# Optimization experiments

Hardware: AMD Instinct MI355X
Metric: run time of the kernel (lower is better)

The kernel has to match this reference:

```python
import jax, jax.numpy as jnp
import numpy as np

N_BATCH = 128   # C: number of PWL channels / generator batch
N_PTS = 32768   # N: samples per channel
K_PWL = 20      # breakpoints per piecewise-linear function
LATENT = 8
HID = 8
EPS = 1e-7


def _mlp(z, W1, b1, W2, b2):
    # torch mlp: Linear -> Tanh -> Linear -> Tanh
    h = jnp.tanh(z @ W1 + b1)
    return jnp.tanh(h @ W2 + b2)


def _normalize01(a):
    # per-row min/max normalization, a: [C, N]
    a = a - a.min(axis=1, keepdims=True)
    return a / a.max(axis=1, keepdims=True)


def _calibrate1d(x, xp, yp):
    # x: [N, C], xp/yp: [C, K]
    N, C = x.shape
    K = xp.shape[1]
    bp = jnp.concatenate([x[:, :, None], jnp.broadcast_to(xp[None], (N, C, K))], axis=2)  # [N,C,K+1]
    order = jnp.argsort(bp, axis=2)                       # [N,C,K+1]
    sorted_bp = jnp.take_along_axis(bp, order, axis=2)
    x_idx = jnp.argmin(order, axis=2)                     # rank of x among breakpoints
    cand = x_idx - 1
    start_idx = jnp.where(x_idx == 0, 1, jnp.where(x_idx == K, K - 2, cand))
    end_idx = jnp.where(start_idx == cand, start_idx + 2, start_idx + 1)
    start_x = jnp.take_along_axis(sorted_bp, start_idx[..., None], axis=2)[..., 0]
    end_x = jnp.take_along_axis(sorted_bp, end_idx[..., None], axis=2)[..., 0]
    start_idx2 = jnp.where(x_idx == 0, 0, jnp.where(x_idx == K, K - 2, cand))
    yp_e = jnp.broadcast_to(yp[None], (N, C, K))
    start_y = jnp.take_along_axis(yp_e, start_idx2[..., None], axis=2)[..., 0]
    end_y = jnp.take_along_axis(yp_e, (start_idx2 + 1)[..., None], axis=2)[..., 0]
    return start_y + (x - start_x) * (end_y - start_y) / (end_x - start_x + EPS)


def setup_inputs() -> dict:
    key = jax.random.key(0)
    ks = jax.random.split(key, 16)
    s = 0.5
    f32 = jnp.float32
    return {
        "zf": jax.random.normal(ks[0], (N_BATCH, LATENT), f32),
        "zx": jax.random.normal(ks[1], (N_BATCH, N_PTS, LATENT), f32),
        "ze": jax.random.normal(ks[2], (N_BATCH, N_PTS, LATENT), f32),
        "Wx1": jax.random.normal(ks[3], (LATENT, HID), f32) * s,
        "bx1": jax.random.normal(ks[4], (HID,), f32) * s,
        "Wx2": jax.random.normal(ks[5], (HID, 1), f32) * s,
        "bx2": jax.random.normal(ks[6], (1,), f32) * s,
        "We1": jax.random.normal(ks[7], (LATENT, HID), f32) * s,
        "be1": jax.random.normal(ks[8], (HID,), f32) * s,
        "We2": jax.random.normal(ks[9], (HID, 1), f32) * s,
        "be2": jax.random.normal(ks[10], (1,), f32) * s,
        "Wf1": jax.random.normal(ks[11], (LATENT, HID), f32) * s,
        "bf1": jax.random.normal(ks[12], (HID,), f32) * s,
        "Wf2": jax.random.normal(ks[13], (HID, K_PWL), f32) * s,
        "bf2": jax.random.normal(ks[14], (K_PWL,), f32) * s,
        "directions": jax.random.randint(ks[15], (N_BATCH,), 0, 2) > 0,
    }


def reference(zf, zx, ze, Wx1, bx1, Wx2, bx2, We1, be1, We2, be2, Wf1, bf1, Wf2, bf2, directions):
    # gen_f: random ascending/descending monotone PWL per channel
    pts = _mlp(zf, Wf1, bf1, Wf2, bf2)                        # [C, K]
    asc = jnp.sort(pts, axis=1)
    yp = jnp.where(directions[:, None], asc, asc[:, ::-1])    # [C, K]
    xp = jnp.broadcast_to(jnp.linspace(0.0, 1.0, K_PWL, dtype=pts.dtype)[None, :], yp.shape)
    # forward_x: cause variable, per-channel normalized to [0,1]
    x = _mlp(zx, Wx1, bx1, Wx2, bx2)[..., 0]                  # [C, N]
    x = _normalize01(x).T                                     # [N, C]
    # forward_e: standardized noise (global mean / unbiased std)
    e = _mlp(ze, We1, be1, We2, be2)[..., 0].T                # [N, C]
    e = (e - e.mean()) / e.std(ddof=1)
    # forward_y
    y = _calibrate1d(x, xp, yp) + 0.1 * e                     # [N, C]
    return y
```

## Files before the change

kernel.cpp:

```cpp
#include <hip/hip_runtime.h>

#define C_CH  128
#define NP    32768
#define K_PWL 20
#define LAT   8
#define HID   8
#define SLOTS 32

__device__ __forceinline__ float fast_tanh(float x) {
    float e = __expf(2.0f * x);
    return 1.0f - 2.0f / (e + 1.0f);
}

__device__ __forceinline__ unsigned fenc(float f) {
    unsigned u = __float_as_uint(f);
    return (u & 0x80000000u) ? ~u : (u | 0x80000000u);
}
__device__ __forceinline__ float fdec(unsigned e) {
    unsigned u = (e & 0x80000000u) ? (e ^ 0x80000000u) : ~e;
    return __uint_as_float(u);
}

__global__ void init_stats(unsigned* cminE, unsigned* cmaxE, double* sums) {
    int t = threadIdx.x;
    if (t < C_CH) { cminE[t] = 0xFFFFFFFFu; cmaxE[t] = 0u; }
    if (t < 2 * SLOTS) sums[t] = 0.0;
}

__global__ void gen_yp(const float* __restrict__ zf,
                       const float* __restrict__ Wf1, const float* __restrict__ bf1,
                       const float* __restrict__ Wf2, const float* __restrict__ bf2,
                       const unsigned char* __restrict__ dirs_raw,
                       float* __restrict__ ypw) {
    int c = threadIdx.x;
    __shared__ int is_i32;
    if (c == 0) {
        const int* di = (const int*)dirs_raw;
        int ok = 1;
        for (int i = 0; i < 32; i++) { int v = di[i]; if (v != 0 && v != 1) ok = 0; }
        is_i32 = ok;
    }
    __syncthreads();
    if (c >= C_CH) return;

    float z[LAT];
    #pragma unroll
    for (int l = 0; l < LAT; l++) z[l] = zf[c * LAT + l];
    float h[HID];
    #pragma unroll
    for (int j = 0; j < HID; j++) {
        float a = bf1[j];
        #pragma unroll
        for (int l = 0; l < LAT; l++) a = fmaf(z[l], Wf1[l * HID + j], a);
        h[j] = fast_tanh(a);
    }
    float p[K_PWL];
    #pragma unroll
    for (int k = 0; k < K_PWL; k++) {
        float a = bf2[k];
        #pragma unroll
        for (int j = 0; j < HID; j++) a = fmaf(h[j], Wf2[j * K_PWL + k], a);
        p[k] = fast_tanh(a);
    }
    for (int i = 1; i < K_PWL; i++) {
        float key = p[i];
        int j = i - 1;
        while (j >= 0 && p[j] > key) { p[j + 1] = p[j]; j--; }
        p[j + 1] = key;
    }
    int dir = is_i32 ? (((const int*)dirs_raw)[c] != 0) : (dirs_raw[c] != 0);
    for (int k = 0; k < K_PWL; k++)
        ypw[c * K_PWL + k] = dir ? p[k] : p[K_PWL - 1 - k];
}

__global__ __launch_bounds__(256)
void pass1(const float* __restrict__ zx, const float* __restrict__ ze,
           const float* __restrict__ Wx1, const float* __restrict__ bx1,
           const float* __restrict__ Wx2, const float* __restrict__ bx2,
           const float* __restrict__ We1, const float* __restrict__ be1,
           const float* __restrict__ We2, const float* __restrict__ be2,
           float* __restrict__ xraw, float* __restrict__ eraw,
           unsigned* __restrict__ cminE, unsigned* __restrict__ cmaxE,
           double* __restrict__ sums) {
    __shared__ float sw[162];
    int t = threadIdx.x;
    if (t < 64)       sw[t] = Wx1[t];
    else if (t < 72)  sw[t] = bx1[t - 64];
    else if (t < 80)  sw[t] = Wx2[t - 72];
    else if (t == 80) sw[80] = bx2[0];
    else if (t < 145) sw[t] = We1[t - 81];
    else if (t < 153) sw[t] = be1[t - 145];
    else if (t < 161) sw[t] = We2[t - 153];
    else if (t == 161) sw[161] = be2[0];
    __syncthreads();

    int c = blockIdx.y;
    int n = blockIdx.x * 256 + t;
    size_t base = ((size_t)c * NP + n) * LAT;

    const float4* zxp = (const float4*)(zx + base);
    float4 a0 = zxp[0], a1 = zxp[1];
    const float4* zep = (const float4*)(ze + base);
    float4 b0 = zep[0], b1 = zep[1];

    float xacc = sw[80];
    #pragma unroll
    for (int j = 0; j < HID; j++) {
        float hh = sw[64 + j];
        hh = fmaf(a0.x, sw[0 * 8 + j], hh);
        hh = fmaf(a0.y, sw[1 * 8 + j], hh);
        hh = fmaf(a0.z, sw[2 * 8 + j], hh);
        hh = fmaf(a0.w, sw[3 * 8 + j], hh);
        hh = fmaf(a1.x, sw[4 * 8 + j], hh);
        hh = fmaf(a1.y, sw[5 * 8 + j], hh);
        hh = fmaf(a1.z, sw[6 * 8 + j], hh);
        hh = fmaf(a1.w, sw[7 * 8 + j], hh);
        xacc = fmaf(fast_tanh(hh), sw[72 + j], xacc);
    }
    float xv = fast_tanh(xacc);

    float eacc = sw[161];
    #pragma unroll
    for (int j = 0; j < HID; j++) {
        float hh = sw[145 + j];
        hh = fmaf(b0.x, sw[81 + 0 * 8 + j], hh);
        hh = fmaf(b0.y, sw[81 + 1 * 8 + j], hh);
        hh = fmaf(b0.z, sw[81 + 2 * 8 + j], hh);
        hh = fmaf(b0.w, sw[81 + 3 * 8 + j], hh);
        hh = fmaf(b1.x, sw[81 + 4 * 8 + j], hh);
        hh = fmaf(b1.y, sw[81 + 5 * 8 + j], hh);
        hh = fmaf(b1.z, sw[81 + 6 * 8 + j], hh);
        hh = fmaf(b1.w, sw[81 + 7 * 8 + j], hh);
        eacc = fmaf(fast_tanh(hh), sw[153 + j], eacc);
    }
    float ev = fast_tanh(eacc);

    xraw[(size_t)c * NP + n] = xv;
    eraw[(size_t)c * NP + n] = ev;

    float mn = xv, mx = xv, s = ev, s2 = ev * ev;
    #pragma unroll
    for (int o = 32; o > 0; o >>= 1) {
        mn = fminf(mn, __shfl_down(mn, o));
        mx = fmaxf(mx, __shfl_down(mx, o));
        s += __shfl_down(s, o);
        s2 += __shfl_down(s2, o);
    }
    __shared__ float rmn[4], rmx[4], rs[4], rs2[4];
    int wave = t >> 6, lane = t & 63;
    if (lane == 0) { rmn[wave] = mn; rmx[wave] = mx; rs[wave] = s; rs2[wave] = s2; }
    __syncthreads();
    if (t == 0) {
        for (int w = 1; w < 4; w++) {
            mn = fminf(mn, rmn[w]); mx = fmaxf(mx, rmx[w]);
            s += rs[w]; s2 += rs2[w];
        }
        atomicMin(&cminE[c], fenc(mn));
        atomicMax(&cmaxE[c], fenc(mx));
        int slot = (blockIdx.x + blockIdx.y) & (SLOTS - 1);
        atomicAdd(&sums[2 * slot], (double)s);
        atomicAdd(&sums[2 * slot + 1], (double)s2);
    }
}

__global__ __launch_bounds__(256)
void pass2(const float* __restrict__ xraw, const float* __restrict__ eraw,
           const float* __restrict__ ypw,
           const unsigned* __restrict__ cminE, const unsigned* __restrict__ cmaxE,
           const double* __restrict__ sums,
           float* __restrict__ out) {
    __shared__ float ytile[C_CH * 33];
    __shared__ float syp[C_CH * K_PWL];
    __shared__ float smin[C_CH], sinv[C_CH];
    __shared__ float sstat[2];

    int t = threadIdx.x;
    for (int i = t; i < C_CH * K_PWL; i += 256) syp[i] = ypw[i];
    if (t < C_CH) {
        float mn = fdec(cminE[t]);
        float mx = fdec(cmaxE[t]);
        smin[t] = mn;
        sinv[t] = 1.0f / (mx - mn);
    }
    if (t == 0) {
        double s = 0.0, s2 = 0.0;
        for (int i = 0; i < SLOTS; i++) { s += sums[2 * i]; s2 += sums[2 * i + 1]; }
        double M = (double)C_CH * NP;
        double mean = s / M;
        double var = (s2 - s * s / M) / (M - 1.0);
        sstat[0] = (float)mean;
        sstat[1] = (float)(0.1 / sqrt(var));
    }
    __syncthreads();

    const float INV_DENOM = 1.0f / (1.0f / 19.0f + 1e-7f);
    float mean = sstat[0], escale = sstat[1];
    int n0 = blockIdx.x * 32;

    #pragma unroll
    for (int i = 0; i < 16; i++) {
        int idx = i * 256 + t;
        int c = idx >> 5;
        int j = idx & 31;
        size_t g = (size_t)c * NP + (n0 + j);
        float x = xraw[g];
        float e = eraw[g];
        float xn = (x - smin[c]) * sinv[c];
        int seg = (int)floorf(xn * 19.0f);
        seg = max(0, min(18, seg));
        float y0 = syp[c * K_PWL + seg];
        float y1 = syp[c * K_PWL + seg + 1];
        float y = fmaf((xn - (float)seg * (1.0f / 19.0f)) * INV_DENOM, y1 - y0, y0);
        y = fmaf(e - mean, escale, y);
        ytile[c * 33 + j] = y;
    }
    __syncthreads();
    #pragma unroll
    for (int i = 0; i < 16; i++) {
        int idx = i * 256 + t;
        int j = idx >> 7;
        int c = idx & 127;
        out[(size_t)(n0 + j) * C_CH + c] = ytile[c * 33 + j];
    }
}

extern "C" void kernel_launch(void* const* d_in, const int* in_sizes, int n_in,
                              void* d_out, int out_size, void* d_ws, size_t ws_size,
                              hipStream_t stream) {
    const float* zf  = (const float*)d_in[0];
    const float* zx  = (const float*)d_in[1];
    const float* ze  = (const float*)d_in[2];
    const float* Wx1 = (const float*)d_in[3];
    const float* bx1 = (const float*)d_in[4];
    const float* Wx2 = (const float*)d_in[5];
    const float* bx2 = (const float*)d_in[6];
    const float* We1 = (const float*)d_in[7];
    const float* be1 = (const float*)d_in[8];
    const float* We2 = (const float*)d_in[9];
    const float* be2 = (const float*)d_in[10];
    const float* Wf1 = (const float*)d_in[11];
    const float* bf1 = (const float*)d_in[12];
    const float* Wf2 = (const float*)d_in[13];
    const float* bf2 = (const float*)d_in[14];
    const unsigned char* dirs = (const unsigned char*)d_in[15];

    float* xraw = (float*)d_ws;
    float* eraw = xraw + (size_t)C_CH * NP;
    float* ypw  = eraw + (size_t)C_CH * NP;
    unsigned* cminE = (unsigned*)(ypw + C_CH * K_PWL);
    unsigned* cmaxE = cminE + C_CH;
    double* sums = (double*)(cmaxE + C_CH);

    hipLaunchKernelGGL(init_stats, dim3(1), dim3(256), 0, stream,
                       cminE, cmaxE, sums);
    hipLaunchKernelGGL(gen_yp, dim3(1), dim3(128), 0, stream,
                       zf, Wf1, bf1, Wf2, bf2, dirs, ypw);
    hipLaunchKernelGGL(pass1, dim3(NP / 256, C_CH), dim3(256), 0, stream,
                       zx, ze, Wx1, bx1, Wx2, bx2, We1, be1, We2, be2,
                       xraw, eraw, cminE, cmaxE, sums);
    hipLaunchKernelGGL(pass2, dim3(NP / 32), dim3(256), 0, stream,
                       xraw, eraw, ypw, cminE, cmaxE, sums, (float*)d_out);
}
```

Baseline: 367.1 us.

## Process four points per thread in pass1, merge init kernels, use rcp

```diff
diff --git a/kernel.cpp b/kernel.cpp
--- a/kernel.cpp
+++ b/kernel.cpp
@@ -6,10 +6,11 @@
 #define LAT   8
 #define HID   8
 #define SLOTS 32
+#define PTS   4
 
 __device__ __forceinline__ float fast_tanh(float x) {
     float e = __expf(2.0f * x);
-    return 1.0f - 2.0f / (e + 1.0f);
+    return fmaf(-2.0f, __builtin_amdgcn_rcpf(e + 1.0f), 1.0f);
 }
 
 __device__ __forceinline__ unsigned fenc(float f) {
@@ -21,27 +22,26 @@
     return __uint_as_float(u);
 }
 
-__global__ void init_stats(unsigned* cminE, unsigned* cmaxE, double* sums) {
+__global__ void prep(const float* __restrict__ zf,
+                     const float* __restrict__ Wf1, const float* __restrict__ bf1,
+                     const float* __restrict__ Wf2, const float* __restrict__ bf2,
+                     const unsigned char* __restrict__ dirs_raw,
+                     float* __restrict__ ypw,
+                     unsigned* cminE, unsigned* cmaxE, double* sums) {
     int t = threadIdx.x;
     if (t < C_CH) { cminE[t] = 0xFFFFFFFFu; cmaxE[t] = 0u; }
     if (t < 2 * SLOTS) sums[t] = 0.0;
-}
-
-__global__ void gen_yp(const float* __restrict__ zf,
-                       const float* __restrict__ Wf1, const float* __restrict__ bf1,
-                       const float* __restrict__ Wf2, const float* __restrict__ bf2,
-                       const unsigned char* __restrict__ dirs_raw,
-                       float* __restrict__ ypw) {
-    int c = threadIdx.x;
+
     __shared__ int is_i32;
-    if (c == 0) {
+    if (t == 0) {
         const int* di = (const int*)dirs_raw;
         int ok = 1;
         for (int i = 0; i < 32; i++) { int v = di[i]; if (v != 0 && v != 1) ok = 0; }
         is_i32 = ok;
     }
     __syncthreads();
-    if (c >= C_CH) return;
+    if (t >= C_CH) return;
+    int c = t;
 
     float z[LAT];
     #pragma unroll
@@ -95,50 +95,66 @@
     __syncthreads();
 
     int c = blockIdx.y;
-    int n = blockIdx.x * 256 + t;
-    size_t base = ((size_t)c * NP + n) * LAT;
-
-    const float4* zxp = (const float4*)(zx + base);
-    float4 a0 = zxp[0], a1 = zxp[1];
-    const float4* zep = (const float4*)(ze + base);
-    float4 b0 = zep[0], b1 = zep[1];
-
-    float xacc = sw[80];
-    #pragma unroll
-    for (int j = 0; j < HID; j++) {
-        float hh = sw[64 + j];
-        hh = fmaf(a0.x, sw[0 * 8 + j], hh);
-        hh = fmaf(a0.y, sw[1 * 8 + j], hh);
-        hh = fmaf(a0.z, sw[2 * 8 + j], hh);
-        hh = fmaf(a0.w, sw[3 * 8 + j], hh);
-        hh = fmaf(a1.x, sw[4 * 8 + j], hh);
-        hh = fmaf(a1.y, sw[5 * 8 + j], hh);
-        hh = fmaf(a1.z, sw[6 * 8 + j], hh);
-        hh = fmaf(a1.w, sw[7 * 8 + j], hh);
-        xacc = fmaf(fast_tanh(hh), sw[72 + j], xacc);
-    }
-    float xv = fast_tanh(xacc);
-
-    float eacc = sw[161];
-    #pragma unroll
-    for (int j = 0; j < HID; j++) {
-        float hh = sw[145 + j];
-        hh = fmaf(b0.x, sw[81 + 0 * 8 + j], hh);
-        hh = fmaf(b0.y, sw[81 + 1 * 8 + j], hh);
-        hh = fmaf(b0.z, sw[81 + 2 * 8 + j], hh);
-        hh = fmaf(b0.w, sw[81 + 3 * 8 + j], hh);
-        hh = fmaf(b1.x, sw[81 + 4 * 8 + j], hh);
-        hh = fmaf(b1.y, sw[81 + 5 * 8 + j], hh);
-        hh = fmaf(b1.z, sw[81 + 6 * 8 + j], hh);
-        hh = fmaf(b1.w, sw[81 + 7 * 8 + j], hh);
-        eacc = fmaf(fast_tanh(hh), sw[153 + j], eacc);
-    }
-    float ev = fast_tanh(eacc);
-
-    xraw[(size_t)c * NP + n] = xv;
-    eraw[(size_t)c * NP + n] = ev;
-
-    float mn = xv, mx = xv, s = ev, s2 = ev * ev;
+    int n0 = blockIdx.x * (256 * PTS) + t;
+    size_t row = (size_t)c * NP;
+    const float4* zx4 = (const float4*)(zx + row * LAT);
+    const float4* ze4 = (const float4*)(ze + row * LAT);
+
+    float4 ax[PTS][2], ae[PTS][2];
+    #pragma unroll
+    for (int k = 0; k < PTS; k++) {
+        int n = n0 + k * 256;
+        ax[k][0] = zx4[2 * n];  ax[k][1] = zx4[2 * n + 1];
+        ae[k][0] = ze4[2 * n];  ae[k][1] = ze4[2 * n + 1];
+    }
+
+    float xv[PTS], ev[PTS];
+    #pragma unroll
+    for (int k = 0; k < PTS; k++) {
+        float acc = sw[80];
+        #pragma unroll
+        for (int j = 0; j < HID; j++) {
+            float hh = sw[64 + j];
+            hh = fmaf(ax[k][0].x, sw[0 * 8 + j], hh);
+            hh = fmaf(ax[k][0].y, sw[1 * 8 + j], hh);
+            hh = fmaf(ax[k][0].z, sw[2 * 8 + j], hh);
+            hh = fmaf(ax[k][0].w, sw[3 * 8 + j], hh);
+            hh = fmaf(ax[k][1].x, sw[4 * 8 + j], hh);
+            hh = fmaf(ax[k][1].y, sw[5 * 8 + j], hh);
+            hh = fmaf(ax[k][1].z, sw[6 * 8 + j], hh);
+            hh = fmaf(ax[k][1].w, sw[7 * 8 + j], hh);
+            acc = fmaf(fast_tanh(hh), sw[72 + j], acc);
+        }
+        xv[k] = fast_tanh(acc);
+    }
+    #pragma unroll
+    for (int k = 0; k < PTS; k++) {
+        float acc = sw[161];
+        #pragma unroll
+        for (int j = 0; j < HID; j++) {
+            float hh = sw[145 + j];
+            hh = fmaf(ae[k][0].x, sw[81 + 0 * 8 + j], hh);
+            hh = fmaf(ae[k][0].y, sw[81 + 1 * 8 + j], hh);
+            hh = fmaf(ae[k][0].z, sw[81 + 2 * 8 + j], hh);
+            hh = fmaf(ae[k][0].w, sw[81 + 3 * 8 + j], hh);
+            hh = fmaf(ae[k][1].x, sw[81 + 4 * 8 + j], hh);
+            hh = fmaf(ae[k][1].y, sw[81 + 5 * 8 + j], hh);
+            hh = fmaf(ae[k][1].z, sw[81 + 6 * 8 + j], hh);
+            hh = fmaf(ae[k][1].w, sw[81 + 7 * 8 + j], hh);
+            acc = fmaf(fast_tanh(hh), sw[153 + j], acc);
+        }
+        ev[k] = fast_tanh(acc);
+    }
+
+    float mn = xv[0], mx = xv[0], s = 0.f, s2 = 0.f;
+    #pragma unroll
+    for (int k = 0; k < PTS; k++) {
+        xraw[row + n0 + k * 256] = xv[k];
+        eraw[row + n0 + k * 256] = ev[k];
+        mn = fminf(mn, xv[k]); mx = fmaxf(mx, xv[k]);
+        s += ev[k]; s2 += ev[k] * ev[k];
+    }
+
     #pragma unroll
     for (int o = 32; o > 0; o >>= 1) {
         mn = fminf(mn, __shfl_down(mn, o));
@@ -180,7 +196,7 @@
         float mn = fdec(cminE[t]);
         float mx = fdec(cmaxE[t]);
         smin[t] = mn;
-        sinv[t] = 1.0f / (mx - mn);
+        sinv[t] = __builtin_amdgcn_rcpf(mx - mn);
     }
     if (t == 0) {
         double s = 0.0, s2 = 0.0;
@@ -251,11 +267,9 @@
     unsigned* cmaxE = cminE + C_CH;
     double* sums = (double*)(cmaxE + C_CH);
 
-    hipLaunchKernelGGL(init_stats, dim3(1), dim3(256), 0, stream,
-                       cminE, cmaxE, sums);
-    hipLaunchKernelGGL(gen_yp, dim3(1), dim3(128), 0, stream,
-                       zf, Wf1, bf1, Wf2, bf2, dirs, ypw);
-    hipLaunchKernelGGL(pass1, dim3(NP / 256, C_CH), dim3(256), 0, stream,
+    hipLaunchKernelGGL(prep, dim3(1), dim3(256), 0, stream,
+                       zf, Wf1, bf1, Wf2, bf2, dirs, ypw, cminE, cmaxE, sums);
+    hipLaunchKernelGGL(pass1, dim3(NP / (256 * PTS), C_CH), dim3(256), 0, stream,
                        zx, ze, Wx1, bx1, Wx2, bx2, We1, be1, We2, be2,
                        xraw, eraw, cminE, cmaxE, sums);
     hipLaunchKernelGGL(pass2, dim3(NP / 32), dim3(256), 0, stream,
```

New measurement: 344.2 us. 1.07x faster.

## Coalesce latent loads via shared transpose, pack x/e as float2, merge prep kernels

Applied to the files above, without the earlier changes.

```diff
diff --git a/kernel.cpp b/kernel.cpp
--- a/kernel.cpp
+++ b/kernel.cpp
@@ -9,7 +9,7 @@
 
 __device__ __forceinline__ float fast_tanh(float x) {
     float e = __expf(2.0f * x);
-    return 1.0f - 2.0f / (e + 1.0f);
+    return fmaf(-2.0f, __builtin_amdgcn_rcpf(e + 1.0f), 1.0f);
 }
 
 __device__ __forceinline__ unsigned fenc(float f) {
@@ -21,27 +21,26 @@
     return __uint_as_float(u);
 }
 
-__global__ void init_stats(unsigned* cminE, unsigned* cmaxE, double* sums) {
+__global__ void prep(const float* __restrict__ zf,
+                     const float* __restrict__ Wf1, const float* __restrict__ bf1,
+                     const float* __restrict__ Wf2, const float* __restrict__ bf2,
+                     const unsigned char* __restrict__ dirs_raw,
+                     float* __restrict__ ypw,
+                     unsigned* cminE, unsigned* cmaxE, double* sums) {
     int t = threadIdx.x;
     if (t < C_CH) { cminE[t] = 0xFFFFFFFFu; cmaxE[t] = 0u; }
     if (t < 2 * SLOTS) sums[t] = 0.0;
-}
-
-__global__ void gen_yp(const float* __restrict__ zf,
-                       const float* __restrict__ Wf1, const float* __restrict__ bf1,
-                       const float* __restrict__ Wf2, const float* __restrict__ bf2,
-                       const unsigned char* __restrict__ dirs_raw,
-                       float* __restrict__ ypw) {
-    int c = threadIdx.x;
+
     __shared__ int is_i32;
-    if (c == 0) {
+    if (t == 0) {
         const int* di = (const int*)dirs_raw;
         int ok = 1;
         for (int i = 0; i < 32; i++) { int v = di[i]; if (v != 0 && v != 1) ok = 0; }
         is_i32 = ok;
     }
     __syncthreads();
-    if (c >= C_CH) return;
+    if (t >= C_CH) return;
+    int c = t;
 
     float z[LAT];
     #pragma unroll
@@ -73,16 +72,19 @@
         ypw[c * K_PWL + k] = dir ? p[k] : p[K_PWL - 1 - k];
 }
 
-__global__ __launch_bounds__(256)
+__global__ __launch_bounds__(256, 8)
 void pass1(const float* __restrict__ zx, const float* __restrict__ ze,
            const float* __restrict__ Wx1, const float* __restrict__ bx1,
            const float* __restrict__ Wx2, const float* __restrict__ bx2,
            const float* __restrict__ We1, const float* __restrict__ be1,
            const float* __restrict__ We2, const float* __restrict__ be2,
-           float* __restrict__ xraw, float* __restrict__ eraw,
+           float2* __restrict__ xe,
            unsigned* __restrict__ cminE, unsigned* __restrict__ cmaxE,
            double* __restrict__ sums) {
+    __shared__ float szx[LAT][256];
+    __shared__ float sze[LAT][256];
     __shared__ float sw[162];
+
     int t = threadIdx.x;
     if (t < 64)       sw[t] = Wx1[t];
     else if (t < 72)  sw[t] = bx1[t - 64];
@@ -92,51 +94,56 @@
     else if (t < 153) sw[t] = be1[t - 145];
     else if (t < 161) sw[t] = We2[t - 153];
     else if (t == 161) sw[161] = be2[0];
-    __syncthreads();
 
     int c = blockIdx.y;
-    int n = blockIdx.x * 256 + t;
-    size_t base = ((size_t)c * NP + n) * LAT;
-
-    const float4* zxp = (const float4*)(zx + base);
-    float4 a0 = zxp[0], a1 = zxp[1];
-    const float4* zep = (const float4*)(ze + base);
-    float4 b0 = zep[0], b1 = zep[1];
+    size_t row = (size_t)c * NP;
+    int tile0 = blockIdx.x * 256;
+    const float4* zx4 = (const float4*)(zx + (row + tile0) * LAT);
+    const float4* ze4 = (const float4*)(ze + (row + tile0) * LAT);
+
+    float4 vx0 = zx4[t];
+    float4 vx1 = zx4[256 + t];
+    float4 ve0 = ze4[t];
+    float4 ve1 = ze4[256 + t];
+
+    {
+        int q = t, p = q >> 1, l0 = (q & 1) * 4;
+        szx[l0 + 0][p] = vx0.x; szx[l0 + 1][p] = vx0.y;
+        szx[l0 + 2][p] = vx0.z; szx[l0 + 3][p] = vx0.w;
+        sze[l0 + 0][p] = ve0.x; sze[l0 + 1][p] = ve0.y;
+        sze[l0 + 2][p] = ve0.z; sze[l0 + 3][p] = ve0.w;
+    }
+    {
+        int q = 256 + t, p = q >> 1, l0 = (q & 1) * 4;
+        szx[l0 + 0][p] = vx1.x; szx[l0 + 1][p] = vx1.y;
+        szx[l0 + 2][p] = vx1.z; szx[l0 + 3][p] = vx1.w;
+        sze[l0 + 0][p] = ve1.x; sze[l0 + 1][p] = ve1.y;
+        sze[l0 + 2][p] = ve1.z; sze[l0 + 3][p] = ve1.w;
+    }
+    __syncthreads();
+
+    float ix[LAT], ie[LAT];
+    #pragma unroll
+    for (int l = 0; l < LAT; l++) { ix[l] = szx[l][t]; ie[l] = sze[l][t]; }
 
     float xacc = sw[80];
+    float eacc = sw[161];
     #pragma unroll
     for (int j = 0; j < HID; j++) {
-        float hh = sw[64 + j];
-        hh = fmaf(a0.x, sw[0 * 8 + j], hh);
-        hh = fmaf(a0.y, sw[1 * 8 + j], hh);
-        hh = fmaf(a0.z, sw[2 * 8 + j], hh);
-        hh = fmaf(a0.w, sw[3 * 8 + j], hh);
-        hh = fmaf(a1.x, sw[4 * 8 + j], hh);
-        hh = fmaf(a1.y, sw[5 * 8 + j], hh);
-        hh = fmaf(a1.z, sw[6 * 8 + j], hh);
-        hh = fmaf(a1.w, sw[7 * 8 + j], hh);
-        xacc = fmaf(fast_tanh(hh), sw[72 + j], xacc);
+        float hx = sw[64 + j];
+        float he = sw[145 + j];
+        #pragma unroll
+        for (int l = 0; l < LAT; l++) {
+            hx = fmaf(ix[l], sw[l * 8 + j], hx);
+            he = fmaf(ie[l], sw[81 + l * 8 + j], he);
+        }
+        xacc = fmaf(fast_tanh(hx), sw[72 + j], xacc);
+        eacc = fmaf(fast_tanh(he), sw[153 + j], eacc);
     }
     float xv = fast_tanh(xacc);
-
-    float eacc = sw[161];
-    #pragma unroll
-    for (int j = 0; j < HID; j++) {
-        float hh = sw[145 + j];
-        hh = fmaf(b0.x, sw[81 + 0 * 8 + j], hh);
-        hh = fmaf(b0.y, sw[81 + 1 * 8 + j], hh);
-        hh = fmaf(b0.z, sw[81 + 2 * 8 + j], hh);
-        hh = fmaf(b0.w, sw[81 + 3 * 8 + j], hh);
-        hh = fmaf(b1.x, sw[81 + 4 * 8 + j], hh);
-        hh = fmaf(b1.y, sw[81 + 5 * 8 + j], hh);
-        hh = fmaf(b1.z, sw[81 + 6 * 8 + j], hh);
-        hh = fmaf(b1.w, sw[81 + 7 * 8 + j], hh);
-        eacc = fmaf(fast_tanh(hh), sw[153 + j], eacc);
-    }
     float ev = fast_tanh(eacc);
 
-    xraw[(size_t)c * NP + n] = xv;
-    eraw[(size_t)c * NP + n] = ev;
+    xe[row + tile0 + t] = make_float2(xv, ev);
 
     float mn = xv, mx = xv, s = ev, s2 = ev * ev;
     #pragma unroll
@@ -164,8 +171,7 @@
 }
 
 __global__ __launch_bounds__(256)
-void pass2(const float* __restrict__ xraw, const float* __restrict__ eraw,
-           const float* __restrict__ ypw,
+void pass2(const float2* __restrict__ xe, const float* __restrict__ ypw,
            const unsigned* __restrict__ cminE, const unsigned* __restrict__ cmaxE,
            const double* __restrict__ sums,
            float* __restrict__ out) {
@@ -180,7 +186,7 @@
         float mn = fdec(cminE[t]);
         float mx = fdec(cmaxE[t]);
         smin[t] = mn;
-        sinv[t] = 1.0f / (mx - mn);
+        sinv[t] = __builtin_amdgcn_rcpf(mx - mn);
     }
     if (t == 0) {
         double s = 0.0, s2 = 0.0;
@@ -202,16 +208,14 @@
         int idx = i * 256 + t;
         int c = idx >> 5;
         int j = idx & 31;
-        size_t g = (size_t)c * NP + (n0 + j);
-        float x = xraw[g];
-        float e = eraw[g];
-        float xn = (x - smin[c]) * sinv[c];
+        float2 v = xe[(size_t)c * NP + (n0 + j)];
+        float xn = (v.x - smin[c]) * sinv[c];
         int seg = (int)floorf(xn * 19.0f);
         seg = max(0, min(18, seg));
         float y0 = syp[c * K_PWL + seg];
         float y1 = syp[c * K_PWL + seg + 1];
         float y = fmaf((xn - (float)seg * (1.0f / 19.0f)) * INV_DENOM, y1 - y0, y0);
-        y = fmaf(e - mean, escale, y);
+        y = fmaf(v.y - mean, escale, y);
         ytile[c * 33 + j] = y;
     }
     __syncthreads();
@@ -244,20 +248,17 @@
     const float* bf2 = (const float*)d_in[14];
     const unsigned char* dirs = (const unsigned char*)d_in[15];
 
-    float* xraw = (float*)d_ws;
-    float* eraw = xraw + (size_t)C_CH * NP;
-    float* ypw  = eraw + (size_t)C_CH * NP;
+    float2* xe  = (float2*)d_ws;
+    float*  ypw = (float*)(xe + (size_t)C_CH * NP);
     unsigned* cminE = (unsigned*)(ypw + C_CH * K_PWL);
     unsigned* cmaxE = cminE + C_CH;
     double* sums = (double*)(cmaxE + C_CH);
 
-    hipLaunchKernelGGL(init_stats, dim3(1), dim3(256), 0, stream,
-                       cminE, cmaxE, sums);
-    hipLaunchKernelGGL(gen_yp, dim3(1), dim3(128), 0, stream,
-                       zf, Wf1, bf1, Wf2, bf2, dirs, ypw);
+    hipLaunchKernelGGL(prep, dim3(1), dim3(256), 0, stream,
+                       zf, Wf1, bf1, Wf2, bf2, dirs, ypw, cminE, cmaxE, sums);
     hipLaunchKernelGGL(pass1, dim3(NP / 256, C_CH), dim3(256), 0, stream,
                        zx, ze, Wx1, bx1, Wx2, bx2, We1, be1, We2, be2,
-                       xraw, eraw, cminE, cmaxE, sums);
+                       xe, cminE, cmaxE, sums);
     hipLaunchKernelGGL(pass2, dim3(NP / 32), dim3(256), 0, stream,
-                       xraw, eraw, ypw, cminE, cmaxE, sums, (float*)d_out);
-}
+                       xe, ypw, cminE, cmaxE, sums, (float*)d_out);
+}
```

After: 366.8 us. No clear change (-0.1%).
